# Performance work log

Measured on AMD Instinct MI355X. Metric: run time of the kernel, lower is better.

The kernel has to match this reference:

```python
import jax, jax.numpy as jnp
import numpy as np

N_NODES = 50000
N_EDGES = 1000000


def _edge_conv(x, src, dst, W, b, n_nodes):
    """PyG EdgeConv: msg = nn(cat([x_i, x_j - x_i])), aggr=max over incoming edges."""
    xi = x[dst]                      # [E, C] target features
    xj = x[src]                      # [E, C] source features
    m = jnp.concatenate([xi, xj - xi], axis=-1)          # [E, 2C]
    m = jax.nn.relu(m @ W + b)                           # [E, C_out]
    out = jax.ops.segment_max(m, dst, num_segments=n_nodes)  # [N, C_out]
    # empty segments produce -inf; PyG fills with 0
    return jnp.where(jnp.isfinite(out), out, 0.0)


def setup_inputs() -> dict:
    key = jax.random.key(0)
    ks = jax.random.split(key, 12)
    x = jax.random.normal(ks[0], (N_NODES, 3), dtype=jnp.float32)
    edge_index = jax.random.randint(ks[1], (2, N_EDGES), 0, N_NODES, dtype=jnp.int64)

    def lin(k, fan_in, fan_out):
        s = 1.0 / np.sqrt(fan_in)
        kw, kb = jax.random.split(k)
        W = jax.random.uniform(kw, (fan_in, fan_out), jnp.float32, -s, s)
        b = jax.random.uniform(kb, (fan_out,), jnp.float32, -s, s)
        return W, b

    W1, b1 = lin(ks[2], 6, 64)       # conv1 MLP([3*2, 64])
    W2, b2 = lin(ks[3], 128, 128)    # conv2 MLP([64*2, 128])
    W3, b3 = lin(ks[4], 256, 512)    # conv3 MLP([128*2, 512])
    W4, b4 = lin(ks[5], 512, 256)    # lin1 MLP([512, 256])
    W5, b5 = lin(ks[6], 256, 3)      # lin1 final Linear(256, 3)
    return {"x": x, "edge_index": edge_index,
            "W1": W1, "b1": b1, "W2": W2, "b2": b2, "W3": W3, "b3": b3,
            "W4": W4, "b4": b4, "W5": W5, "b5": b5}


def reference(x, edge_index, W1, b1, W2, b2, W3, b3, W4, b4, W5, b5):
    src = edge_index[0]  # x_j
    dst = edge_index[1]  # x_i (aggregation target)
    n = x.shape[0]
    x1 = _edge_conv(x, src, dst, W1, b1, n)    # [N, 64]
    x2 = _edge_conv(x1, src, dst, W2, b2, n)   # [N, 128]
    x3 = _edge_conv(x2, src, dst, W3, b3, n)   # [N, 512]
    x4 = jax.nn.relu(x3 @ W4 + b4) @ W5 + b5   # [N, 3]
    return x + x4
```

## Files before the change

### kernel.cpp

```cpp
#include <hip/hip_runtime.h>

static constexpr int NN = 50000;
static constexpr int NE = 1000000;

typedef short bf16x8 __attribute__((ext_vector_type(8)));
typedef float f32x4 __attribute__((ext_vector_type(4)));
typedef unsigned short u16x2 __attribute__((ext_vector_type(2)));

__device__ inline float bf2f_raw(unsigned short u) {
    return __uint_as_float(((unsigned int)u) << 16);
}
__device__ inline unsigned short f2bf(float f) {
    unsigned int u = __float_as_uint(f);
    u += 0x7fffu + ((u >> 16) & 1u);
    return (unsigned short)(u >> 16);
}
__device__ inline unsigned short f2bfs(float f) {
    unsigned short b = f2bf(f);
    return (b & 0x8000u) ? (unsigned short)(~b) : (unsigned short)(b | 0x8000u);
}
__device__ inline float unsrt2f(unsigned short v) {
    unsigned short b = (v & 0x8000u) ? (unsigned short)(v ^ 0x8000u)
                                     : (unsigned short)(~v);
    return bf2f_raw(b);
}
__device__ inline unsigned int pkmax(unsigned int a, unsigned int b) {
    u16x2 r = __builtin_elementwise_max(__builtin_bit_cast(u16x2, a),
                                        __builtin_bit_cast(u16x2, b));
    return __builtin_bit_cast(unsigned int, r);
}
__device__ inline uint4 pkmax4(uint4 a, uint4 b) {
    a.x = pkmax(a.x, b.x); a.y = pkmax(a.y, b.y);
    a.z = pkmax(a.z, b.z); a.w = pkmax(a.w, b.w);
    return a;
}
__device__ inline unsigned int pack2(float f0, float f1) {
    return (unsigned int)f2bf(f0) | ((unsigned int)f2bf(f1) << 16);
}
__device__ inline unsigned int addrelu2t(unsigned int a, unsigned int t) {
    float t0 = unsrt2f((unsigned short)(t & 0xffffu));
    float t1 = unsrt2f((unsigned short)(t >> 16));
    float f0 = fmaxf(bf2f_raw((unsigned short)(a & 0xffffu)) + t0, 0.f);
    float f1 = fmaxf(bf2f_raw((unsigned short)(a >> 16)) + t1, 0.f);
    return pack2(f0, f1);
}


__global__ void setup_kernel(const float* __restrict__ x, const float* __restrict__ W1,
                             const float* __restrict__ b1, const float* __restrict__ b5,
                             const float* __restrict__ W2, const float* __restrict__ W3,
                             const float* __restrict__ W4,
                             unsigned short* __restrict__ as1, float* __restrict__ out,
                             int* __restrict__ deg, int* __restrict__ cursor,
                             unsigned short* __restrict__ Bt2,
                             unsigned short* __restrict__ Bt3,
                             unsigned short* __restrict__ W4t) {
    int t = blockIdx.x * blockDim.x + threadIdx.x;
    if (t < NN * 128) {
        int i = t >> 7, c = t & 127;
        float x0 = x[i * 3 + 0], x1 = x[i * 3 + 1], x2 = x[i * 3 + 2];
        if (c < 64) {
            float v = x0 * (W1[c] - W1[192 + c]) + x1 * (W1[64 + c] - W1[256 + c]) +
                      x2 * (W1[128 + c] - W1[320 + c]) + b1[c];
            as1[t] = f2bf(v);
        } else {
            int cs = c - 64;
            float v = x0 * W1[192 + cs] + x1 * W1[256 + cs] + x2 * W1[320 + cs];
            as1[t] = f2bfs(v);
        }
        return;
    }
    t -= NN * 128;
    if (t < NN * 3) { out[t] = x[t] + b5[t % 3]; return; }
    t -= NN * 3;
    if (t < NN) { deg[t] = 0; return; }
    t -= NN;
    if (t < NN) { cursor[t] = 0; return; }
    t -= NN;
    if (t < 8192) {
        int k = t / 128, c = t % 128;
        float wt = W2[k * 128 + c];
        float wb = W2[(64 + k) * 128 + c];
        Bt2[c * 64 + k] = f2bf(wt - wb);
        Bt2[(128 + c) * 64 + k] = f2bf(wb);
        return;
    }
    t -= 8192;
    if (t < 65536) {
        int k = t / 512, c = t % 512;
        float wt = W3[k * 512 + c];
        float wb = W3[(128 + k) * 512 + c];
        Bt3[c * 128 + k] = f2bf(wt - wb);
        Bt3[(512 + c) * 128 + k] = f2bf(wb);
        return;
    }
    t -= 65536;
    if (t < 131072) {
        int k = t / 256, n = t % 256;
        W4t[n * 512 + k] = f2bf(W4[k * 256 + n]);
    }
}


__global__ void hist_kernel(const int* __restrict__ dst, int* __restrict__ deg) {
    int e = blockIdx.x * blockDim.x + threadIdx.x;
    if (e < NE) atomicAdd(&deg[dst[e]], 1);
}

__global__ __launch_bounds__(1024) void scan_kernel(const int* __restrict__ deg,
                                                    int* __restrict__ rowstart) {
    __shared__ int wave_sums[16];
    constexpr int CH = (NN + 1023) / 1024;
    int tid = threadIdx.x;
    int lane = tid & 63;
    int wave = tid >> 6;
    int base = tid * CH;
    int vals[CH];
    int sum = 0;
    #pragma unroll
    for (int i = 0; i < CH; ++i) {
        int idx = base + i;
        vals[i] = (idx < NN) ? deg[idx] : 0;
        sum += vals[i];
    }
    int x = sum;
    #pragma unroll
    for (int off = 1; off < 64; off <<= 1) {
        int y = __shfl_up(x, off);
        if (lane >= off) x += y;
    }
    if (lane == 63) wave_sums[wave] = x;
    __syncthreads();
    if (wave == 0 && lane < 16) {
        int s = wave_sums[lane];
        #pragma unroll
        for (int off = 1; off < 16; off <<= 1) {
            int y = __shfl_up(s, off);
            if (lane >= off) s += y;
        }
        wave_sums[lane] = s;
    }
    __syncthreads();
    int run = (wave ? wave_sums[wave - 1] : 0) + x - sum;
    #pragma unroll
    for (int i = 0; i < CH; ++i) {
        int idx = base + i;
        if (idx < NN) rowstart[idx] = run;
        run += vals[i];
    }
    if (tid == 1023) rowstart[NN] = run;
}

__global__ void scatter_kernel(const int* __restrict__ src, const int* __restrict__ dst,
                               const int* __restrict__ rowstart, int* __restrict__ cursor,
                               int* __restrict__ csr) {
    int e = blockIdx.x * blockDim.x + threadIdx.x;
    if (e < NE) {
        int d = dst[e];
        int pos = atomicAdd(&cursor[d], 1);
        csr[rowstart[d] + pos] = src[e];
    }
}


__global__ __launch_bounds__(256) void edge_fused_conv1_kernel(
    const unsigned short* __restrict__ as, const int* __restrict__ rowstart,
    const int* __restrict__ csr, unsigned short* __restrict__ x1) {
    int wid = (blockIdx.x * 256 + threadIdx.x) >> 6;
    int lane = threadIdx.x & 63;
    if (wid >= NN) return;
    int e0 = __builtin_amdgcn_readfirstlane(rowstart[wid]);
    int e1 = __builtin_amdgcn_readfirstlane(rowstart[wid + 1]);
    int nedge = e1 - e0;
    unsigned int mA = 0u, mB = 0u;
    if (nedge > 0) {
        int last = nedge - 1;
        for (int e = 0; e < nedge; e += 16) {
            int jj[16];
            #pragma unroll
            for (int k = 0; k < 16; ++k) {
                int idx = e + k; if (idx > last) idx = last;
                jj[k] = __builtin_amdgcn_readfirstlane(csr[e0 + idx]);
            }
            unsigned int v[16];
            #pragma unroll
            for (int k = 0; k < 16; ++k)
                v[k] = *(const unsigned short*)(as + (size_t)jj[k] * 128 + 64 + lane);
            #pragma unroll
            for (int k = 0; k < 16; ++k) {
                if (k & 1) mB = mB > v[k] ? mB : v[k];
                else       mA = mA > v[k] ? mA : v[k];
            }
        }
    }
    unsigned int m = mA > mB ? mA : mB;
    unsigned short a = as[(size_t)wid * 128 + lane];
    float t = unsrt2f((unsigned short)m);
    float f = fmaxf(bf2f_raw(a) + t, 0.f);
    x1[(size_t)wid * 64 + lane] = f2bf(f);
}


__global__ __launch_bounds__(256) void edge_fused128_kernel(
    const unsigned short* __restrict__ as, const int* __restrict__ rowstart,
    const int* __restrict__ csr, unsigned short* __restrict__ xout) {
    int wid = (blockIdx.x * 256 + threadIdx.x) >> 6;
    int lane = threadIdx.x & 63;
    if (wid >= NN) return;
    int e0 = __builtin_amdgcn_readfirstlane(rowstart[wid]);
    int e1 = __builtin_amdgcn_readfirstlane(rowstart[wid + 1]);
    int nedge = e1 - e0;
    unsigned int mA = 0u, mB = 0u;
    if (nedge > 0) {
        int last = nedge - 1;
        for (int e = 0; e < nedge; e += 16) {
            int jj[16];
            #pragma unroll
            for (int k = 0; k < 16; ++k) {
                int idx = e + k; if (idx > last) idx = last;
                jj[k] = __builtin_amdgcn_readfirstlane(csr[e0 + idx]);
            }
            unsigned int v[16];
            #pragma unroll
            for (int k = 0; k < 16; ++k)
                v[k] = *(const unsigned int*)(as + (size_t)jj[k] * 256 + 128 + lane * 2);
            #pragma unroll
            for (int k = 0; k < 16; ++k) {
                if (k & 1) mB = pkmax(mB, v[k]);
                else       mA = pkmax(mA, v[k]);
            }
        }
    }
    unsigned int t = pkmax(mA, mB);
    unsigned int av = *(const unsigned int*)(as + (size_t)wid * 256 + lane * 2);
    *(unsigned int*)(xout + (size_t)wid * 128 + lane * 2) = addrelu2t(av, t);
}


__global__ __launch_bounds__(256) void ef512_w5_kernel(
    const unsigned short* __restrict__ as, const int* __restrict__ rowstart,
    const int* __restrict__ csr, const unsigned short* __restrict__ W4t,
    const float* __restrict__ b4, const float* __restrict__ W5,
    float* __restrict__ out) {
    __shared__ __align__(16) unsigned short X[16][520];
    int wave = threadIdx.x >> 6, lane = threadIdx.x & 63;
    int tilebase = blockIdx.x * 16;

    for (int i = 0; i < 4; ++i) {
        int node = tilebase + wave * 4 + i;
        int e0 = __builtin_amdgcn_readfirstlane(rowstart[node]);
        int e1 = __builtin_amdgcn_readfirstlane(rowstart[node + 1]);
        int nedge = e1 - e0;
        uint4 mA = make_uint4(0u, 0u, 0u, 0u), mB = make_uint4(0u, 0u, 0u, 0u);
        if (nedge > 0) {
            int last = nedge - 1;
            for (int e = 0; e < nedge; e += 8) {
                int jj[8];
                #pragma unroll
                for (int k = 0; k < 8; ++k) {
                    int idx = e + k; if (idx > last) idx = last;
                    jj[k] = __builtin_amdgcn_readfirstlane(csr[e0 + idx]);
                }
                uint4 v[8];
                #pragma unroll
                for (int k = 0; k < 8; ++k)
                    v[k] = *(const uint4*)(as + (size_t)jj[k] * 1024 + 512 + lane * 8);
                #pragma unroll
                for (int k = 0; k < 8; ++k) {
                    if (k & 1) mB = pkmax4(mB, v[k]);
                    else       mA = pkmax4(mA, v[k]);
                }
            }
        }
        uint4 m = pkmax4(mA, mB);
        uint4 av = *(const uint4*)(as + (size_t)node * 1024 + lane * 8);
        uint4 o;
        o.x = addrelu2t(av.x, m.x);
        o.y = addrelu2t(av.y, m.y);
        o.z = addrelu2t(av.z, m.z);
        o.w = addrelu2t(av.w, m.w);
        *(uint4*)&X[wave * 4 + i][lane * 8] = o;
    }
    __syncthreads();

    int quad = lane >> 4, l16 = lane & 15;
    int colbase = wave * 64;
    f32x4 acc4[4] = {};
    for (int kc = 0; kc < 16; ++kc) {
        bf16x8 afr = *(const bf16x8*)&X[l16][kc * 32 + quad * 8];
        #pragma unroll
        for (int nt = 0; nt < 4; ++nt) {
            int col = colbase + nt * 16 + l16;
            bf16x8 bfr = *(const bf16x8*)&W4t[(size_t)col * 512 + kc * 32 + quad * 8];
            acc4[nt] = __builtin_amdgcn_mfma_f32_16x16x32_bf16(afr, bfr, acc4[nt], 0, 0, 0);
        }
    }
    float b4v[4], w5r[4][3];
    #pragma unroll
    for (int nt = 0; nt < 4; ++nt) {
        int col = colbase + nt * 16 + l16;
        b4v[nt] = b4[col];
        w5r[nt][0] = W5[col * 3 + 0];
        w5r[nt][1] = W5[col * 3 + 1];
        w5r[nt][2] = W5[col * 3 + 2];
    }
    #pragma unroll
    for (int r = 0; r < 4; ++r) {
        int row = tilebase + quad * 4 + r;
        float p0 = 0.f, p1 = 0.f, p2 = 0.f;
        #pragma unroll
        for (int nt = 0; nt < 4; ++nt) {
            float h = fmaxf(acc4[nt][r] + b4v[nt], 0.f);
            p0 += h * w5r[nt][0];
            p1 += h * w5r[nt][1];
            p2 += h * w5r[nt][2];
        }
        #pragma unroll
        for (int m = 8; m; m >>= 1) {
            p0 += __shfl_xor(p0, m);
            p1 += __shfl_xor(p1, m);
            p2 += __shfl_xor(p2, m);
        }
        if (l16 == 0) {
            atomicAdd(&out[row * 3 + 0], p0);
            atomicAdd(&out[row * 3 + 1], p1);
            atomicAdd(&out[row * 3 + 2], p2);
        }
    }
}


template<int K, int NT>
__global__ __launch_bounds__(256) void mfma_gemm_nloop_kernel(
    const unsigned short* __restrict__ A, const unsigned short* __restrict__ Bt,
    const float* __restrict__ bias, int bias_n,
    unsigned short* __restrict__ C, int M) {
    constexpr int KC = K / 32;
    constexpr int N = NT * 128;
    __shared__ __align__(16) unsigned short Asl[KC][128 * 40];
    __shared__ __align__(16) unsigned short Bsl[128 * 40];
    int tid = threadIdx.x;
    int mbase = blockIdx.x * 128;
    int wave = tid >> 6, lane = tid & 63;
    int wm = (wave >> 1) * 64, wn = (wave & 1) * 64;
    int quad = lane >> 4, l16 = lane & 15;

    #pragma unroll
    for (int c = tid; c < KC * 512; c += 256) {
        int kc = c >> 9, rem = c & 511;
        int r = rem >> 2, kk = (rem & 3) * 8;
        uint4 va = make_uint4(0u, 0u, 0u, 0u);
        int gr = mbase + r;
        if (gr < M) va = *(const uint4*)&A[(size_t)gr * K + kc * 32 + kk];
        *(uint4*)&Asl[kc][r * 40 + kk] = va;
    }

    for (int nt = 0; nt < NT; ++nt) {
        int nbase = nt * 128;
        f32x4 acc[4][4] = {};
        for (int kc = 0; kc < KC; ++kc) {
            __syncthreads();
            #pragma unroll
            for (int h = 0; h < 2; ++h) {
                int c = tid + h * 256;
                int r = c >> 2, kk = (c & 3) * 8;
                uint4 vb = *(const uint4*)&Bt[(size_t)(nbase + r) * K + kc * 32 + kk];
                *(uint4*)&Bsl[r * 40 + kk] = vb;
            }
            __syncthreads();
            bf16x8 af[4], bfr[4];
            #pragma unroll
            for (int tt = 0; tt < 4; ++tt) {
                af[tt]  = *(const bf16x8*)&Asl[kc][(wm + tt * 16 + l16) * 40 + quad * 8];
                bfr[tt] = *(const bf16x8*)&Bsl[(wn + tt * 16 + l16) * 40 + quad * 8];
            }
            #pragma unroll
            for (int mt = 0; mt < 4; ++mt)
                #pragma unroll
                for (int ntt = 0; ntt < 4; ++ntt)
                    acc[mt][ntt] = __builtin_amdgcn_mfma_f32_16x16x32_bf16(
                        af[mt], bfr[ntt], acc[mt][ntt], 0, 0, 0);
        }
        #pragma unroll
        for (int mt = 0; mt < 4; ++mt) {
            #pragma unroll
            for (int r = 0; r < 4; ++r) {
                int row = mbase + wm + mt * 16 + quad * 4 + r;
                if (row >= M) continue;
                #pragma unroll
                for (int ntt = 0; ntt < 4; ++ntt) {
                    int col = nbase + wn + ntt * 16 + l16;
                    float v = acc[mt][ntt][r];
                    unsigned short o;
                    if (col < bias_n) o = f2bf(v + bias[col]);
                    else o = f2bfs(v);
                    C[(size_t)row * N + col] = o;
                }
            }
        }
    }
}

__global__ void fallback_copy_kernel(const float* __restrict__ x, float* __restrict__ out) {
    int t = blockIdx.x * blockDim.x + threadIdx.x;
    if (t < NN * 3) out[t] = x[t];
}


extern "C" void kernel_launch(void* const* d_in, const int* in_sizes, int n_in,
                              void* d_out, int out_size, void* d_ws, size_t ws_size,
                              hipStream_t stream) {
    const float* x  = (const float*)d_in[0];
    const int*   ei = (const int*)d_in[1];
    const float* W1 = (const float*)d_in[2];
    const float* b1 = (const float*)d_in[3];
    const float* W2 = (const float*)d_in[4];
    const float* b2 = (const float*)d_in[5];
    const float* W3 = (const float*)d_in[6];
    const float* b3 = (const float*)d_in[7];
    const float* W4 = (const float*)d_in[8];
    const float* b4 = (const float*)d_in[9];
    const float* W5 = (const float*)d_in[10];
    const float* b5 = (const float*)d_in[11];
    float* out = (float*)d_out;

    char* p = (char*)d_ws;
    auto alloc = [&](size_t bytes) -> void* {
        void* r = (void*)p;
        p += (bytes + 255) & ~(size_t)255;
        return r;
    };
    int* deg      = (int*)alloc((size_t)NN * 4);
    int* rowstart = (int*)alloc((size_t)(NN + 1) * 4);
    int* cursor   = (int*)alloc((size_t)NN * 4);
    int* csr      = (int*)alloc((size_t)NE * 4);
    unsigned short* Bt2 = (unsigned short*)alloc(256 * 64 * 2);
    unsigned short* Bt3 = (unsigned short*)alloc(1024 * 128 * 2);
    unsigned short* W4t = (unsigned short*)alloc(256 * 512 * 2);
    unsigned short* x1 = (unsigned short*)alloc((size_t)NN * 64 * 2);
    unsigned short* x2 = (unsigned short*)alloc((size_t)NN * 128 * 2);
    unsigned short* as_slab = (unsigned short*)alloc((size_t)NN * 1024 * 2);
    size_t need = (size_t)(p - (char*)d_ws);
    if (ws_size < need) {
        fallback_copy_kernel<<<(NN * 3 + 255) / 256, 256, 0, stream>>>(x, out);
        return;
    }

    const int* src = ei;
    const int* dst = ei + NE;

    constexpr int SETUP_T = NN * 128 + NN * 3 + NN + NN + 8192 + 65536 + 131072;
    setup_kernel<<<(SETUP_T + 255) / 256, 256, 0, stream>>>(
        x, W1, b1, b5, W2, W3, W4, as_slab, out, deg, cursor, Bt2, Bt3, W4t);

    hist_kernel<<<(NE + 255) / 256, 256, 0, stream>>>(dst, deg);
    scan_kernel<<<1, 1024, 0, stream>>>(deg, rowstart);
    scatter_kernel<<<(NE + 255) / 256, 256, 0, stream>>>(src, dst, rowstart, cursor, csr);

    edge_fused_conv1_kernel<<<12500, 256, 0, stream>>>(as_slab, rowstart, csr, x1);

    mfma_gemm_nloop_kernel<64, 2><<<391, 256, 0, stream>>>(
        x1, Bt2, b2, 128, as_slab, NN);
    edge_fused128_kernel<<<12500, 256, 0, stream>>>(as_slab, rowstart, csr, x2);

    mfma_gemm_nloop_kernel<128, 8><<<391, 256, 0, stream>>>(
        x2, Bt3, b3, 512, as_slab, NN);

    ef512_w5_kernel<<<NN / 16, 256, 0, stream>>>(
        as_slab, rowstart, csr, W4t, b4, W5, out);
}
```

Baseline: 599.7 us.

## Bucket CSR neighbors by source block and gather in bucket-major order across waves

Builds a two-level CSR where each destination's incoming edges are grouped into 49 buckets by source index (src>>10). A per-node bucket scan replaces the single cursor. The gather kernels walk buckets in order, and the 512-wide kernel interleaves its four nodes per bucket, so concurrent gathers hit nearby source rows and get better cache locality. The cost is a 49x larger histogram and scan array, extra atomics, an added scan kernel, and serial per-edge loops that no longer batch 16 independent loads for memory-level parallelism.

```diff
diff --git a/kernel.cpp b/kernel.cpp
--- a/kernel.cpp
+++ b/kernel.cpp
@@ -2,6 +2,8 @@
 
 static constexpr int NN = 50000;
 static constexpr int NE = 1000000;
+static constexpr int NB = 49;
+static constexpr int BSHIFT = 10;
 
 typedef short bf16x8 __attribute__((ext_vector_type(8)));
 typedef float f32x4 __attribute__((ext_vector_type(4)));
@@ -51,7 +53,7 @@
                              const float* __restrict__ W2, const float* __restrict__ W3,
                              const float* __restrict__ W4,
                              unsigned short* __restrict__ as1, float* __restrict__ out,
-                             int* __restrict__ deg, int* __restrict__ cursor,
+                             int* __restrict__ deg, int* __restrict__ deg_b,
                              unsigned short* __restrict__ Bt2,
                              unsigned short* __restrict__ Bt3,
                              unsigned short* __restrict__ W4t) {
@@ -75,8 +77,8 @@
     t -= NN * 3;
     if (t < NN) { deg[t] = 0; return; }
     t -= NN;
-    if (t < NN) { cursor[t] = 0; return; }
-    t -= NN;
+    if (t < NN * NB) { deg_b[t] = 0; return; }
+    t -= NN * NB;
     if (t < 8192) {
         int k = t / 128, c = t % 128;
         float wt = W2[k * 128 + c];
@@ -102,9 +104,14 @@
 }
 
 
-__global__ void hist_kernel(const int* __restrict__ dst, int* __restrict__ deg) {
+__global__ void hist_kernel(const int* __restrict__ src, const int* __restrict__ dst,
+                            int* __restrict__ deg, int* __restrict__ deg_b) {
     int e = blockIdx.x * blockDim.x + threadIdx.x;
-    if (e < NE) atomicAdd(&deg[dst[e]], 1);
+    if (e < NE) {
+        int d = dst[e];
+        atomicAdd(&deg[d], 1);
+        atomicAdd(&deg_b[d * NB + (src[e] >> BSHIFT)], 1);
+    }
 }
 
 __global__ __launch_bounds__(1024) void scan_kernel(const int* __restrict__ deg,
@@ -151,49 +158,67 @@
     if (tid == 1023) rowstart[NN] = run;
 }
 
+__global__ __launch_bounds__(256) void scan_b_kernel(const int* __restrict__ rowstart,
+                                                     int* __restrict__ deg_b ,
+                                                     int* __restrict__ rsb) {
+    int wid = (blockIdx.x * 256 + threadIdx.x) >> 6;
+    int lane = threadIdx.x & 63;
+    if (wid >= NN) return;
+    int d = (lane < NB) ? deg_b[wid * NB + lane] : 0;
+    int x = d;
+    #pragma unroll
+    for (int off = 1; off < 64; off <<= 1) {
+        int y = __shfl_up(x, off);
+        if (lane >= off) x += y;
+    }
+    int v = rowstart[wid] + (x - d);
+    if (lane < NB) {
+        rsb[wid * NB + lane] = v;
+        deg_b[wid * NB + lane] = v;
+    }
+}
+
 __global__ void scatter_kernel(const int* __restrict__ src, const int* __restrict__ dst,
-                               const int* __restrict__ rowstart, int* __restrict__ cursor,
-                               int* __restrict__ csr) {
+                               int* __restrict__ cursor_b, int* __restrict__ csr) {
     int e = blockIdx.x * blockDim.x + threadIdx.x;
     if (e < NE) {
-        int d = dst[e];
-        int pos = atomicAdd(&cursor[d], 1);
-        csr[rowstart[d] + pos] = src[e];
+        int d = dst[e], s = src[e];
+        int pos = atomicAdd(&cursor_b[d * NB + (s >> BSHIFT)], 1);
+        csr[pos] = s;
     }
 }
 
 
 __global__ __launch_bounds__(256) void edge_fused_conv1_kernel(
     const unsigned short* __restrict__ as, const int* __restrict__ rowstart,
-    const int* __restrict__ csr, unsigned short* __restrict__ x1) {
+    const int* __restrict__ rsb, const int* __restrict__ csr,
+    unsigned short* __restrict__ x1) {
     int wid = (blockIdx.x * 256 + threadIdx.x) >> 6;
     int lane = threadIdx.x & 63;
     if (wid >= NN) return;
     int e0 = __builtin_amdgcn_readfirstlane(rowstart[wid]);
     int e1 = __builtin_amdgcn_readfirstlane(rowstart[wid + 1]);
-    int nedge = e1 - e0;
-    unsigned int mA = 0u, mB = 0u;
-    if (nedge > 0) {
-        int last = nedge - 1;
-        for (int e = 0; e < nedge; e += 16) {
-            int jj[16];
-            #pragma unroll
-            for (int k = 0; k < 16; ++k) {
-                int idx = e + k; if (idx > last) idx = last;
-                jj[k] = __builtin_amdgcn_readfirstlane(csr[e0 + idx]);
-            }
-            unsigned int v[16];
-            #pragma unroll
-            for (int k = 0; k < 16; ++k)
-                v[k] = *(const unsigned short*)(as + (size_t)jj[k] * 128 + 64 + lane);
-            #pragma unroll
-            for (int k = 0; k < 16; ++k) {
-                if (k & 1) mB = mB > v[k] ? mB : v[k];
-                else       mA = mA > v[k] ? mA : v[k];
-            }
-        }
-    }
-    unsigned int m = mA > mB ? mA : mB;
+    int ne = e1 - e0;
+    unsigned int m = 0u;
+    if (ne > 0 && ne <= 64) {
+        int csrv = csr[e0 + (lane < ne ? lane : 0)];
+        int rsbv = (lane < NB) ? rsb[wid * NB + lane] : e1;
+        for (int b = 0; b < NB; ++b) {
+            int s_ = __builtin_amdgcn_readlane(rsbv, b);
+            int t_ = __builtin_amdgcn_readlane(rsbv, b + 1);
+            for (int e = s_; e < t_; ++e) {
+                int j = __builtin_amdgcn_readlane(csrv, e - e0);
+                unsigned int v = *(const unsigned short*)(as + (size_t)j * 128 + 64 + lane);
+                m = m > v ? m : v;
+            }
+        }
+    } else if (ne > 64) {
+        for (int e = e0; e < e1; ++e) {
+            int j = __builtin_amdgcn_readfirstlane(csr[e]);
+            unsigned int v = *(const unsigned short*)(as + (size_t)j * 128 + 64 + lane);
+            m = m > v ? m : v;
+        }
+    }
     unsigned short a = as[(size_t)wid * 128 + lane];
     float t = unsrt2f((unsigned short)m);
     float f = fmaxf(bf2f_raw(a) + t, 0.f);
@@ -203,82 +228,94 @@
 
 __global__ __launch_bounds__(256) void edge_fused128_kernel(
     const unsigned short* __restrict__ as, const int* __restrict__ rowstart,
-    const int* __restrict__ csr, unsigned short* __restrict__ xout) {
+    const int* __restrict__ rsb, const int* __restrict__ csr,
+    unsigned short* __restrict__ xout) {
     int wid = (blockIdx.x * 256 + threadIdx.x) >> 6;
     int lane = threadIdx.x & 63;
     if (wid >= NN) return;
     int e0 = __builtin_amdgcn_readfirstlane(rowstart[wid]);
     int e1 = __builtin_amdgcn_readfirstlane(rowstart[wid + 1]);
-    int nedge = e1 - e0;
-    unsigned int mA = 0u, mB = 0u;
-    if (nedge > 0) {
-        int last = nedge - 1;
-        for (int e = 0; e < nedge; e += 16) {
-            int jj[16];
-            #pragma unroll
-            for (int k = 0; k < 16; ++k) {
-                int idx = e + k; if (idx > last) idx = last;
-                jj[k] = __builtin_amdgcn_readfirstlane(csr[e0 + idx]);
-            }
-            unsigned int v[16];
-            #pragma unroll
-            for (int k = 0; k < 16; ++k)
-                v[k] = *(const unsigned int*)(as + (size_t)jj[k] * 256 + 128 + lane * 2);
-            #pragma unroll
-            for (int k = 0; k < 16; ++k) {
-                if (k & 1) mB = pkmax(mB, v[k]);
-                else       mA = pkmax(mA, v[k]);
-            }
-        }
-    }
-    unsigned int t = pkmax(mA, mB);
+    int ne = e1 - e0;
+    unsigned int m = 0u;
+    if (ne > 0 && ne <= 64) {
+        int csrv = csr[e0 + (lane < ne ? lane : 0)];
+        int rsbv = (lane < NB) ? rsb[wid * NB + lane] : e1;
+        for (int b = 0; b < NB; ++b) {
+            int s_ = __builtin_amdgcn_readlane(rsbv, b);
+            int t_ = __builtin_amdgcn_readlane(rsbv, b + 1);
+            for (int e = s_; e < t_; ++e) {
+                int j = __builtin_amdgcn_readlane(csrv, e - e0);
+                unsigned int v = *(const unsigned int*)(as + (size_t)j * 256 + 128 + lane * 2);
+                m = pkmax(m, v);
+            }
+        }
+    } else if (ne > 64) {
+        for (int e = e0; e < e1; ++e) {
+            int j = __builtin_amdgcn_readfirstlane(csr[e]);
+            unsigned int v = *(const unsigned int*)(as + (size_t)j * 256 + 128 + lane * 2);
+            m = pkmax(m, v);
+        }
+    }
     unsigned int av = *(const unsigned int*)(as + (size_t)wid * 256 + lane * 2);
-    *(unsigned int*)(xout + (size_t)wid * 128 + lane * 2) = addrelu2t(av, t);
+    *(unsigned int*)(xout + (size_t)wid * 128 + lane * 2) = addrelu2t(av, m);
 }
 
 
 __global__ __launch_bounds__(256) void ef512_w5_kernel(
     const unsigned short* __restrict__ as, const int* __restrict__ rowstart,
-    const int* __restrict__ csr, const unsigned short* __restrict__ W4t,
+    const int* __restrict__ rsb, const int* __restrict__ csr,
+    const unsigned short* __restrict__ W4t,
     const float* __restrict__ b4, const float* __restrict__ W5,
     float* __restrict__ out) {
     __shared__ __align__(16) unsigned short X[16][520];
     int wave = threadIdx.x >> 6, lane = threadIdx.x & 63;
     int tilebase = blockIdx.x * 16;
-
+    int node0 = tilebase + wave * 4;
+
+    int eS[4], eE[4], csrv[4], rsbv[4];
+    uint4 m[4];
+    bool big = false;
+    #pragma unroll
     for (int i = 0; i < 4; ++i) {
-        int node = tilebase + wave * 4 + i;
-        int e0 = __builtin_amdgcn_readfirstlane(rowstart[node]);
-        int e1 = __builtin_amdgcn_readfirstlane(rowstart[node + 1]);
-        int nedge = e1 - e0;
-        uint4 mA = make_uint4(0u, 0u, 0u, 0u), mB = make_uint4(0u, 0u, 0u, 0u);
-        if (nedge > 0) {
-            int last = nedge - 1;
-            for (int e = 0; e < nedge; e += 8) {
-                int jj[8];
-                #pragma unroll
-                for (int k = 0; k < 8; ++k) {
-                    int idx = e + k; if (idx > last) idx = last;
-                    jj[k] = __builtin_amdgcn_readfirstlane(csr[e0 + idx]);
+        eS[i] = __builtin_amdgcn_readfirstlane(rowstart[node0 + i]);
+        eE[i] = __builtin_amdgcn_readfirstlane(rowstart[node0 + i + 1]);
+        int ne = eE[i] - eS[i];
+        big = big || (ne > 64);
+        csrv[i] = csr[(ne > 0 ? eS[i] : 0) + (lane < ne ? lane : 0)];
+        rsbv[i] = (lane < NB) ? rsb[(node0 + i) * NB + lane] : eE[i];
+        m[i] = make_uint4(0u, 0u, 0u, 0u);
+    }
+    if (!big) {
+        for (int b = 0; b < NB; ++b) {
+            #pragma unroll
+            for (int i = 0; i < 4; ++i) {
+                int s_ = __builtin_amdgcn_readlane(rsbv[i], b);
+                int t_ = __builtin_amdgcn_readlane(rsbv[i], b + 1);
+                for (int e = s_; e < t_; ++e) {
+                    int j = __builtin_amdgcn_readlane(csrv[i], e - eS[i]);
+                    uint4 v = *(const uint4*)(as + (size_t)j * 1024 + 512 + lane * 8);
+                    m[i] = pkmax4(m[i], v);
                 }
-                uint4 v[8];
-                #pragma unroll
-                for (int k = 0; k < 8; ++k)
-                    v[k] = *(const uint4*)(as + (size_t)jj[k] * 1024 + 512 + lane * 8);
-                #pragma unroll
-                for (int k = 0; k < 8; ++k) {
-                    if (k & 1) mB = pkmax4(mB, v[k]);
-                    else       mA = pkmax4(mA, v[k]);
-                }
-            }
-        }
-        uint4 m = pkmax4(mA, mB);
-        uint4 av = *(const uint4*)(as + (size_t)node * 1024 + lane * 8);
+            }
+        }
+    } else {
+        #pragma unroll
+        for (int i = 0; i < 4; ++i) {
+            for (int e = eS[i]; e < eE[i]; ++e) {
+                int j = __builtin_amdgcn_readfirstlane(csr[e]);
+                uint4 v = *(const uint4*)(as + (size_t)j * 1024 + 512 + lane * 8);
+                m[i] = pkmax4(m[i], v);
+            }
+        }
+    }
+    #pragma unroll
+    for (int i = 0; i < 4; ++i) {
+        uint4 av = *(const uint4*)(as + (size_t)(node0 + i) * 1024 + lane * 8);
         uint4 o;
-        o.x = addrelu2t(av.x, m.x);
-        o.y = addrelu2t(av.y, m.y);
-        o.z = addrelu2t(av.z, m.z);
-        o.w = addrelu2t(av.w, m.w);
+        o.x = addrelu2t(av.x, m[i].x);
+        o.y = addrelu2t(av.y, m[i].y);
+        o.z = addrelu2t(av.z, m[i].z);
+        o.w = addrelu2t(av.w, m[i].w);
         *(uint4*)&X[wave * 4 + i][lane * 8] = o;
     }
     __syncthreads();
@@ -316,10 +353,10 @@
             p2 += h * w5r[nt][2];
         }
         #pragma unroll
-        for (int m = 8; m; m >>= 1) {
-            p0 += __shfl_xor(p0, m);
-            p1 += __shfl_xor(p1, m);
-            p2 += __shfl_xor(p2, m);
+        for (int mm = 8; mm; mm >>= 1) {
+            p0 += __shfl_xor(p0, mm);
+            p1 += __shfl_xor(p1, mm);
+            p2 += __shfl_xor(p2, mm);
         }
         if (l16 == 0) {
             atomicAdd(&out[row * 3 + 0], p0);
@@ -432,7 +469,8 @@
     };
     int* deg      = (int*)alloc((size_t)NN * 4);
     int* rowstart = (int*)alloc((size_t)(NN + 1) * 4);
-    int* cursor   = (int*)alloc((size_t)NN * 4);
+    int* deg_b    = (int*)alloc((size_t)NN * NB * 4);
+    int* rsb      = (int*)alloc((size_t)NN * NB * 4);
     int* csr      = (int*)alloc((size_t)NE * 4);
     unsigned short* Bt2 = (unsigned short*)alloc(256 * 64 * 2);
     unsigned short* Bt3 = (unsigned short*)alloc(1024 * 128 * 2);
@@ -449,23 +487,24 @@
     const int* src = ei;
     const int* dst = ei + NE;
 
-    constexpr int SETUP_T = NN * 128 + NN * 3 + NN + NN + 8192 + 65536 + 131072;
+    constexpr int SETUP_T = NN * 128 + NN * 3 + NN + NN * NB + 8192 + 65536 + 131072;
     setup_kernel<<<(SETUP_T + 255) / 256, 256, 0, stream>>>(
-        x, W1, b1, b5, W2, W3, W4, as_slab, out, deg, cursor, Bt2, Bt3, W4t);
-
-    hist_kernel<<<(NE + 255) / 256, 256, 0, stream>>>(dst, deg);
+        x, W1, b1, b5, W2, W3, W4, as_slab, out, deg, deg_b, Bt2, Bt3, W4t);
+
+    hist_kernel<<<(NE + 255) / 256, 256, 0, stream>>>(src, dst, deg, deg_b);
     scan_kernel<<<1, 1024, 0, stream>>>(deg, rowstart);
-    scatter_kernel<<<(NE + 255) / 256, 256, 0, stream>>>(src, dst, rowstart, cursor, csr);
-
-    edge_fused_conv1_kernel<<<12500, 256, 0, stream>>>(as_slab, rowstart, csr, x1);
+    scan_b_kernel<<<12500, 256, 0, stream>>>(rowstart, deg_b, rsb);
+    scatter_kernel<<<(NE + 255) / 256, 256, 0, stream>>>(src, dst, deg_b, csr);
+
+    edge_fused_conv1_kernel<<<12500, 256, 0, stream>>>(as_slab, rowstart, rsb, csr, x1);
 
     mfma_gemm_nloop_kernel<64, 2><<<391, 256, 0, stream>>>(
         x1, Bt2, b2, 128, as_slab, NN);
-    edge_fused128_kernel<<<12500, 256, 0, stream>>>(as_slab, rowstart, csr, x2);
+    edge_fused128_kernel<<<12500, 256, 0, stream>>>(as_slab, rowstart, rsb, csr, x2);
 
     mfma_gemm_nloop_kernel<128, 8><<<391, 256, 0, stream>>>(
         x2, Bt3, b3, 512, as_slab, NN);
 
     ef512_w5_kernel<<<NN / 16, 256, 0, stream>>>(
-        as_slab, rowstart, csr, W4t, b4, W5, out);
-}
+        as_slab, rowstart, rsb, csr, W4t, b4, W5, out);
+}
```

Result: slower. 802.9 us (+33.9%).

## Bucket CSR neighbor lists by source index range for gather locality

Applied to the files above, without the earlier changes.

Builds a per-destination histogram over 49 source-index buckets, scans it per node, and scatters edges so that each node's neighbor list is roughly sorted by source index. The aim is better cache locality in the gather-heavy edge-conv kernels, since neighbor rows are fetched in address order. In exchange it adds a 2.45M-entry bucket array to zero, a second atomic in the histogram, and an extra scan kernel.

```diff
diff --git a/kernel.cpp b/kernel.cpp
--- a/kernel.cpp
+++ b/kernel.cpp
@@ -2,6 +2,8 @@
 
 static constexpr int NN = 50000;
 static constexpr int NE = 1000000;
+static constexpr int NB = 49;
+static constexpr int BSHIFT = 10;
 
 typedef short bf16x8 __attribute__((ext_vector_type(8)));
 typedef float f32x4 __attribute__((ext_vector_type(4)));
@@ -51,7 +53,7 @@
                              const float* __restrict__ W2, const float* __restrict__ W3,
                              const float* __restrict__ W4,
                              unsigned short* __restrict__ as1, float* __restrict__ out,
-                             int* __restrict__ deg, int* __restrict__ cursor,
+                             int* __restrict__ deg, int* __restrict__ deg_b,
                              unsigned short* __restrict__ Bt2,
                              unsigned short* __restrict__ Bt3,
                              unsigned short* __restrict__ W4t) {
@@ -75,8 +77,8 @@
     t -= NN * 3;
     if (t < NN) { deg[t] = 0; return; }
     t -= NN;
-    if (t < NN) { cursor[t] = 0; return; }
-    t -= NN;
+    if (t < NN * NB) { deg_b[t] = 0; return; }
+    t -= NN * NB;
     if (t < 8192) {
         int k = t / 128, c = t % 128;
         float wt = W2[k * 128 + c];
@@ -102,9 +104,14 @@
 }
 
 
-__global__ void hist_kernel(const int* __restrict__ dst, int* __restrict__ deg) {
+__global__ void hist_kernel(const int* __restrict__ src, const int* __restrict__ dst,
+                            int* __restrict__ deg, int* __restrict__ deg_b) {
     int e = blockIdx.x * blockDim.x + threadIdx.x;
-    if (e < NE) atomicAdd(&deg[dst[e]], 1);
+    if (e < NE) {
+        int d = dst[e];
+        atomicAdd(&deg[d], 1);
+        atomicAdd(&deg_b[d * NB + (src[e] >> BSHIFT)], 1);
+    }
 }
 
 __global__ __launch_bounds__(1024) void scan_kernel(const int* __restrict__ deg,
@@ -151,14 +158,29 @@
     if (tid == 1023) rowstart[NN] = run;
 }
 
+__global__ __launch_bounds__(256) void scan_b_kernel(const int* __restrict__ rowstart,
+                                                     int* __restrict__ deg_b ) {
+    int wid = (blockIdx.x * 256 + threadIdx.x) >> 6;
+    int lane = threadIdx.x & 63;
+    if (wid >= NN) return;
+    int d = (lane < NB) ? deg_b[wid * NB + lane] : 0;
+    int x = d;
+    #pragma unroll
+    for (int off = 1; off < 64; off <<= 1) {
+        int y = __shfl_up(x, off);
+        if (lane >= off) x += y;
+    }
+    int v = rowstart[wid] + (x - d);
+    if (lane < NB) deg_b[wid * NB + lane] = v;
+}
+
 __global__ void scatter_kernel(const int* __restrict__ src, const int* __restrict__ dst,
-                               const int* __restrict__ rowstart, int* __restrict__ cursor,
-                               int* __restrict__ csr) {
+                               int* __restrict__ cursor_b, int* __restrict__ csr) {
     int e = blockIdx.x * blockDim.x + threadIdx.x;
     if (e < NE) {
-        int d = dst[e];
-        int pos = atomicAdd(&cursor[d], 1);
-        csr[rowstart[d] + pos] = src[e];
+        int d = dst[e], s = src[e];
+        int pos = atomicAdd(&cursor_b[d * NB + (s >> BSHIFT)], 1);
+        csr[pos] = s;
     }
 }
 
@@ -432,7 +454,7 @@
     };
     int* deg      = (int*)alloc((size_t)NN * 4);
     int* rowstart = (int*)alloc((size_t)(NN + 1) * 4);
-    int* cursor   = (int*)alloc((size_t)NN * 4);
+    int* deg_b    = (int*)alloc((size_t)NN * NB * 4);
     int* csr      = (int*)alloc((size_t)NE * 4);
     unsigned short* Bt2 = (unsigned short*)alloc(256 * 64 * 2);
     unsigned short* Bt3 = (unsigned short*)alloc(1024 * 128 * 2);
@@ -449,13 +471,14 @@
     const int* src = ei;
     const int* dst = ei + NE;
 
-    constexpr int SETUP_T = NN * 128 + NN * 3 + NN + NN + 8192 + 65536 + 131072;
+    constexpr int SETUP_T = NN * 128 + NN * 3 + NN + NN * NB + 8192 + 65536 + 131072;
     setup_kernel<<<(SETUP_T + 255) / 256, 256, 0, stream>>>(
-        x, W1, b1, b5, W2, W3, W4, as_slab, out, deg, cursor, Bt2, Bt3, W4t);
-
-    hist_kernel<<<(NE + 255) / 256, 256, 0, stream>>>(dst, deg);
+        x, W1, b1, b5, W2, W3, W4, as_slab, out, deg, deg_b, Bt2, Bt3, W4t);
+
+    hist_kernel<<<(NE + 255) / 256, 256, 0, stream>>>(src, dst, deg, deg_b);
     scan_kernel<<<1, 1024, 0, stream>>>(deg, rowstart);
-    scatter_kernel<<<(NE + 255) / 256, 256, 0, stream>>>(src, dst, rowstart, cursor, csr);
+    scan_b_kernel<<<12500, 256, 0, stream>>>(rowstart, deg_b);
+    scatter_kernel<<<(NE + 255) / 256, 256, 0, stream>>>(src, dst, deg_b, csr);
 
     edge_fused_conv1_kernel<<<12500, 256, 0, stream>>>(as_slab, rowstart, csr, x1);
 
```

Result: slower. 678.9 us (+13.2%).

## Compute conv3 self-term inside final kernel, halve GEMM output slab

Applied to the files above, without the earlier changes.

The conv3 GEMM now writes only the 512-wide neighbor half of the projection, so the slab row size drops to 512. The node's own 512-wide self term is recomputed by MFMA inside the final edge-max/MLP kernel from x2 tiles staged in shared memory. This cuts global write and read traffic for the self half, and the gathered rows shrink, which may help cache hit rates. In exchange each block does extra MFMA work and adds shared-memory staging and barriers.

```diff
diff --git a/kernel.cpp b/kernel.cpp
--- a/kernel.cpp
+++ b/kernel.cpp
@@ -238,14 +238,51 @@
 
 
 __global__ __launch_bounds__(256) void ef512_w5_kernel(
-    const unsigned short* __restrict__ as, const int* __restrict__ rowstart,
-    const int* __restrict__ csr, const unsigned short* __restrict__ W4t,
+    const unsigned short* __restrict__ s3, const unsigned short* __restrict__ x2,
+    const int* __restrict__ rowstart, const int* __restrict__ csr,
+    const unsigned short* __restrict__ Bt3a, const float* __restrict__ b3,
+    const unsigned short* __restrict__ W4t,
     const float* __restrict__ b4, const float* __restrict__ W5,
     float* __restrict__ out) {
     __shared__ __align__(16) unsigned short X[16][520];
-    int wave = threadIdx.x >> 6, lane = threadIdx.x & 63;
+    __shared__ __align__(16) unsigned short x2t[16][136];
+    int tid = threadIdx.x;
+    int wave = tid >> 6, lane = tid & 63;
+    int quad = lane >> 4, l16 = lane & 15;
     int tilebase = blockIdx.x * 16;
 
+    {
+        int row = tid >> 4, seg = tid & 15;
+        uint4 v = *(const uint4*)(x2 + (size_t)(tilebase + row) * 128 + seg * 8);
+        *(uint4*)&x2t[row][seg * 8] = v;
+    }
+    __syncthreads();
+
+    {
+        int colbase = wave * 128;
+        f32x4 acc3[8] = {};
+        #pragma unroll
+        for (int kc = 0; kc < 4; ++kc) {
+            bf16x8 afr = *(const bf16x8*)&x2t[l16][kc * 32 + quad * 8];
+            #pragma unroll
+            for (int nt = 0; nt < 8; ++nt) {
+                int col = colbase + nt * 16 + l16;
+                bf16x8 bfr = *(const bf16x8*)&Bt3a[(size_t)col * 128 + kc * 32 + quad * 8];
+                acc3[nt] = __builtin_amdgcn_mfma_f32_16x16x32_bf16(afr, bfr, acc3[nt], 0, 0, 0);
+            }
+        }
+        #pragma unroll
+        for (int nt = 0; nt < 8; ++nt) {
+            int col = colbase + nt * 16 + l16;
+            float bv = b3[col];
+            #pragma unroll
+            for (int r = 0; r < 4; ++r)
+                X[quad * 4 + r][col] = f2bf(acc3[nt][r] + bv);
+        }
+    }
+    __syncthreads();
+
+    const unsigned short* sb = s3 + (size_t)lane * 8;
     for (int i = 0; i < 4; ++i) {
         int node = tilebase + wave * 4 + i;
         int e0 = __builtin_amdgcn_readfirstlane(rowstart[node]);
@@ -264,7 +301,7 @@
                 uint4 v[8];
                 #pragma unroll
                 for (int k = 0; k < 8; ++k)
-                    v[k] = *(const uint4*)(as + (size_t)jj[k] * 1024 + 512 + lane * 8);
+                    v[k] = *(const uint4*)(sb + (size_t)jj[k] * 512);
                 #pragma unroll
                 for (int k = 0; k < 8; ++k) {
                     if (k & 1) mB = pkmax4(mB, v[k]);
@@ -273,7 +310,7 @@
             }
         }
         uint4 m = pkmax4(mA, mB);
-        uint4 av = *(const uint4*)(as + (size_t)node * 1024 + lane * 8);
+        uint4 av = *(const uint4*)&X[wave * 4 + i][lane * 8];
         uint4 o;
         o.x = addrelu2t(av.x, m.x);
         o.y = addrelu2t(av.y, m.y);
@@ -283,7 +320,6 @@
     }
     __syncthreads();
 
-    int quad = lane >> 4, l16 = lane & 15;
     int colbase = wave * 64;
     f32x4 acc4[4] = {};
     for (int kc = 0; kc < 16; ++kc) {
@@ -439,7 +475,7 @@
     unsigned short* W4t = (unsigned short*)alloc(256 * 512 * 2);
     unsigned short* x1 = (unsigned short*)alloc((size_t)NN * 64 * 2);
     unsigned short* x2 = (unsigned short*)alloc((size_t)NN * 128 * 2);
-    unsigned short* as_slab = (unsigned short*)alloc((size_t)NN * 1024 * 2);
+    unsigned short* as_slab = (unsigned short*)alloc((size_t)NN * 512 * 2);
     size_t need = (size_t)(p - (char*)d_ws);
     if (ws_size < need) {
         fallback_copy_kernel<<<(NN * 3 + 255) / 256, 256, 0, stream>>>(x, out);
@@ -463,9 +499,9 @@
         x1, Bt2, b2, 128, as_slab, NN);
     edge_fused128_kernel<<<12500, 256, 0, stream>>>(as_slab, rowstart, csr, x2);
 
-    mfma_gemm_nloop_kernel<128, 8><<<391, 256, 0, stream>>>(
-        x2, Bt3, b3, 512, as_slab, NN);
+    mfma_gemm_nloop_kernel<128, 4><<<391, 256, 0, stream>>>(
+        x2, Bt3 + 512 * 128, b3, 0, as_slab, NN);
 
     ef512_w5_kernel<<<NN / 16, 256, 0, stream>>>(
-        as_slab, rowstart, csr, W4t, b4, W5, out);
-}
+        as_slab, x2, rowstart, csr, Bt3, b3, W4t, b4, W5, out);
+}
```

Measured after the change: 580.3 us. 1.03x faster.
